# Optimization experiments

Measured on AMD Instinct MI355X. Metric: run time of the kernel, lower is better.

The kernel has to match this reference:

```python
import jax, jax.numpy as jnp
import numpy as np

# dims: B batch, T spikes, X/Y output grid, IN input neurons (weights rows), H hidden neurons
B, T, X, Y = 16, 128, 16, 16
IN_DIM, H_DIM = 256, 64


def setup_inputs() -> dict:
    key = jax.random.key(0)
    k1, k2, k3, k4, k5 = jax.random.split(key, 5)
    inp = {}
    # input only determines batch size in the custom forward (used by backward in torch)
    inp["input"] = jax.random.uniform(k1, (B, IN_DIM, X, Y), jnp.float32) + 0.01
    inp["spikes"] = jax.random.randint(k2, (B, T, X, Y), 0, IN_DIM)
    inp["epsilon_xy"] = jax.random.uniform(k3, (IN_DIM, X, Y), jnp.float32) * 0.1 + 0.01
    inp["epsilon_t_0"] = jax.random.uniform(k4, (T,), jnp.float32) * 0.5 + 0.5
    inp["weights"] = jax.random.uniform(k5, (IN_DIM, H_DIM), jnp.float32) + 1e-3
    inp["h_initial"] = jnp.ones((H_DIM,), jnp.float32) / H_DIM
    inp["forgetting_offset"] = jnp.ones((1,), jnp.float32)
    return inp


def _sbs_hdynamics(spikes, epsilon_xy, epsilon_t_0, weights, h_initial, fo):
    # spikes: [B,T,X,Y] int; weights: [IN,H]; epsilon_xy: [IN,X,Y]; h_initial: [H]
    b, t, x, y = spikes.shape
    h = weights.shape[1]
    xg = jnp.arange(x)[None, :, None]  # broadcast index grids for [B,X,Y] gathers
    yg = jnp.arange(y)[None, None, :]
    fo_per_neuron = fo / h
    h0 = jnp.broadcast_to(h_initial, (b, x, y, h)).astype(weights.dtype)

    def step(h_state, inp):
        sp, eps_t = inp                      # sp: [B,X,Y], eps_t: scalar
        w = weights[sp]                      # [B,X,Y,H] gather of weight rows
        eps = epsilon_xy[sp, xg, yg] * eps_t # [B,X,Y] per-pixel/spike epsilon
        h_temp = h_state * w                 # [B,X,Y,H]
        s = h_temp.sum(axis=-1)              # [B,X,Y]
        safe_s = jnp.where(s > 1e-10, s, 1.0)
        scale = (eps / safe_s)[..., None]
        # h <- (h + eps*h*w/ (h.w) + eps*fo/H) / (1 + eps*(1+fo))  (fo=0 reduces to h/(1+eps))
        upd = (h_state + scale * h_temp + (eps * fo_per_neuron)[..., None]) / (
            1.0 + (eps * (1.0 + fo))[..., None]
        )
        h_new = jnp.where((s > 1e-10)[..., None], upd, h_state)
        return h_new, None

    spikes_t = jnp.transpose(spikes, (1, 0, 2, 3))  # [T,B,X,Y]
    h_final, _ = jax.lax.scan(step, h0, (spikes_t, epsilon_t_0))
    return jnp.transpose(h_final, (0, 3, 1, 2))  # [B,H,X,Y]


def reference(input, spikes, epsilon_xy, epsilon_t_0, weights, h_initial, forgetting_offset):
    fo = forgetting_offset[0]
    return _sbs_hdynamics(spikes, epsilon_xy, epsilon_t_0, weights, h_initial, fo)
```

## Files before the change

kernel.cpp:

```cpp
#include <hip/hip_runtime.h>

#define BB      16
#define TT      128
#define XDIM    16
#define YDIM    16
#define IN_DIM  256
#define H_DIM   64
#define XY      (XDIM*YDIM)


#define DPP_ADD(v, ctrl)                                                      \
    v += __int_as_float(__builtin_amdgcn_update_dpp(                          \
        0, __float_as_int(v), (ctrl), 0xf, 0xf, true))

__global__ __launch_bounds__(256) void sbs_scan_kernel(
    const int*   __restrict__ spikes,
    const float* __restrict__ eps_xy,
    const float* __restrict__ eps_t,
    const float* __restrict__ weights,
    const float* __restrict__ h_init,
    const float* __restrict__ fo_ptr,
    float*       __restrict__ out)
{
    __shared__ int    s_spk[YDIM][TT];
    __shared__ float2 s_P[YDIM][TT];
    __shared__ float  s_out[YDIM][H_DIM];

    const int tid = threadIdx.x;
    const int bi  = blockIdx.x;
    const int b   = bi >> 4;
    const int x   = bi & 15;

    int spv[8];
    #pragma unroll
    for (int k = 0; k < 8; ++k) {
        const int idx = tid + k * 256;
        const int t = idx >> 4, yy = idx & 15;
        const int sp = spikes[(b * TT + t) * XY + x * YDIM + yy];
        spv[k] = sp;
        s_spk[yy][t] = sp;
    }

    const float fo   = fo_ptr[0];
    const float fo1  = 1.0f + fo;
    const float fo_h = fo * (1.0f / (float)H_DIM);

    #pragma unroll
    for (int k = 0; k < 8; ++k) {
        const int idx = tid + k * 256;
        const int t = idx >> 4, yy = idx & 15;
        const float eps = eps_xy[spv[k] * XY + x * YDIM + yy] * eps_t[t];
        const float den = fmaf(eps, fo1, 1.0f);
        float rd = __builtin_amdgcn_rcpf(den);
        rd = fmaf(rd, fmaf(-den, rd, 1.0f), rd);
        s_P[yy][t] = make_float2(rd, eps * rd);
    }
    __syncthreads();

    const int wave = tid >> 6;
    const int lane = tid & 63;
    const int row  = lane >> 4;
    const int il   = lane & 15;
    const int y    = wave * 4 + row;

    const float4* __restrict__ w4 = (const float4*)weights;
    float4 h = ((const float4*)h_init)[il];

    int    sq0 = s_spk[y][3];
    int    sq1 = s_spk[y][4];
    float4 wq0 = w4[s_spk[y][0] * 16 + il];
    float4 wq1 = w4[s_spk[y][1] * 16 + il];
    float4 wq2 = w4[s_spk[y][2] * 16 + il];
    float2 pq0 = s_P[y][0];
    float2 pq1 = s_P[y][1];

    #pragma unroll 4
    for (int t = 0; t < TT; ++t) {
        const int    sq_n = s_spk[y][(t + 5) & (TT - 1)];
        const float4 wq_n = w4[sq0 * 16 + il];
        const float2 pq_n = s_P[y][(t + 2) & (TT - 1)];

        const float ht0 = h.x * wq0.x;
        const float ht1 = h.y * wq0.y;
        const float ht2 = h.z * wq0.z;
        const float ht3 = h.w * wq0.w;
        float r = (ht0 + ht1) + (ht2 + ht3);
        DPP_ADD(r, 0xB1);
        DPP_ADD(r, 0x4E);
        DPP_ADD(r, 0x124);
        DPP_ADD(r, 0x128);
        const float s = r;

        float rs = __builtin_amdgcn_rcpf(s);
        rs = fmaf(rs, fmaf(-s, rs, 1.0f), rs);

        const float rd   = pq0.x;
        const float erd  = pq0.y;
        const float erdf = erd * fo_h;
        const float k2   = erd * rs;
        const float u0 = fmaf(k2, ht0, fmaf(h.x, rd, erdf));
        const float u1 = fmaf(k2, ht1, fmaf(h.y, rd, erdf));
        const float u2 = fmaf(k2, ht2, fmaf(h.z, rd, erdf));
        const float u3 = fmaf(k2, ht3, fmaf(h.w, rd, erdf));
        const bool ok = (s > 1e-10f);
        h.x = ok ? u0 : h.x;
        h.y = ok ? u1 : h.y;
        h.z = ok ? u2 : h.z;
        h.w = ok ? u3 : h.w;

        sq0 = sq1; sq1 = sq_n;
        wq0 = wq1; wq1 = wq2; wq2 = wq_n;
        pq0 = pq1; pq1 = pq_n;
    }

    *(float4*)&s_out[y][4 * il] = h;
    __syncthreads();
    #pragma unroll
    for (int k = 0; k < 4; ++k) {
        const int idx = tid + k * 256;
        const int hh = idx >> 4, yy = idx & 15;
        out[b * (H_DIM * XY) + hh * XY + x * YDIM + yy] = s_out[yy][hh];
    }
}

extern "C" void kernel_launch(void* const* d_in, const int* in_sizes, int n_in,
                              void* d_out, int out_size, void* d_ws, size_t ws_size,
                              hipStream_t stream) {
    const int*   spikes  = (const int*)  d_in[1];
    const float* eps_xy  = (const float*)d_in[2];
    const float* eps_t   = (const float*)d_in[3];
    const float* weights = (const float*)d_in[4];
    const float* h_init  = (const float*)d_in[5];
    const float* fo_ptr  = (const float*)d_in[6];
    float*       out     = (float*)d_out;

    const int grid = BB * XDIM;
    sbs_scan_kernel<<<grid, 256, 0, stream>>>(
        spikes, eps_xy, eps_t, weights, h_init, fo_ptr, out);
}
```

Before: 82.25 us.

## Shorten scan critical path: precompute off-chain terms, drop guard and Newton step

Restructures the per-step update so that everything independent of the reduced sum is computed before the DPP reduction, leaving only one rcp and four FMAs after it. It also removes the Newton refinement of the reciprocal and the s>1e-10 guard, which depends on inputs being positive. In addition it deepens the weight-gather prefetch by one step and pads the shared arrays to avoid bank conflicts. Dropping the guard and refinement slightly changes precision and makes the kernel rely on the sum never being near zero.

```diff
diff --git a/kernel.cpp b/kernel.cpp
--- a/kernel.cpp
+++ b/kernel.cpp
@@ -22,9 +22,9 @@
     const float* __restrict__ fo_ptr,
     float*       __restrict__ out)
 {
-    __shared__ int    s_spk[YDIM][TT];
-    __shared__ float2 s_P[YDIM][TT];
-    __shared__ float  s_out[YDIM][H_DIM];
+    __shared__ int    s_spk[YDIM][TT + 1];
+    __shared__ float2 s_P[YDIM][TT + 1];
+    __shared__ float  s_out[YDIM][H_DIM + 1];
 
     const int tid = threadIdx.x;
     const int bi  = blockIdx.x;
@@ -66,51 +66,54 @@
     const float4* __restrict__ w4 = (const float4*)weights;
     float4 h = ((const float4*)h_init)[il];
 
-    int    sq0 = s_spk[y][3];
-    int    sq1 = s_spk[y][4];
+    int    sq0 = s_spk[y][4];
+    int    sq1 = s_spk[y][5];
     float4 wq0 = w4[s_spk[y][0] * 16 + il];
     float4 wq1 = w4[s_spk[y][1] * 16 + il];
     float4 wq2 = w4[s_spk[y][2] * 16 + il];
+    float4 wq3 = w4[s_spk[y][3] * 16 + il];
     float2 pq0 = s_P[y][0];
     float2 pq1 = s_P[y][1];
+    float2 pq2 = s_P[y][2];
 
     #pragma unroll 4
     for (int t = 0; t < TT; ++t) {
-        const int    sq_n = s_spk[y][(t + 5) & (TT - 1)];
+        const int    sq_n = s_spk[y][(t + 6) & (TT - 1)];
         const float4 wq_n = w4[sq0 * 16 + il];
-        const float2 pq_n = s_P[y][(t + 2) & (TT - 1)];
+        const float2 pq_n = s_P[y][(t + 3) & (TT - 1)];
 
         const float ht0 = h.x * wq0.x;
         const float ht1 = h.y * wq0.y;
         const float ht2 = h.z * wq0.z;
         const float ht3 = h.w * wq0.w;
         float r = (ht0 + ht1) + (ht2 + ht3);
+
+        const float rd   = pq0.x;
+        const float erd  = pq0.y;
+        const float erdf = erd * fo_h;
+        const float eht0 = erd * ht0;
+        const float eht1 = erd * ht1;
+        const float eht2 = erd * ht2;
+        const float eht3 = erd * ht3;
+        const float t30 = fmaf(h.x, rd, erdf);
+        const float t31 = fmaf(h.y, rd, erdf);
+        const float t32 = fmaf(h.z, rd, erdf);
+        const float t33 = fmaf(h.w, rd, erdf);
+
         DPP_ADD(r, 0xB1);
         DPP_ADD(r, 0x4E);
         DPP_ADD(r, 0x124);
         DPP_ADD(r, 0x128);
-        const float s = r;
 
-        float rs = __builtin_amdgcn_rcpf(s);
-        rs = fmaf(rs, fmaf(-s, rs, 1.0f), rs);
-
-        const float rd   = pq0.x;
-        const float erd  = pq0.y;
-        const float erdf = erd * fo_h;
-        const float k2   = erd * rs;
-        const float u0 = fmaf(k2, ht0, fmaf(h.x, rd, erdf));
-        const float u1 = fmaf(k2, ht1, fmaf(h.y, rd, erdf));
-        const float u2 = fmaf(k2, ht2, fmaf(h.z, rd, erdf));
-        const float u3 = fmaf(k2, ht3, fmaf(h.w, rd, erdf));
-        const bool ok = (s > 1e-10f);
-        h.x = ok ? u0 : h.x;
-        h.y = ok ? u1 : h.y;
-        h.z = ok ? u2 : h.z;
-        h.w = ok ? u3 : h.w;
+        const float rs = __builtin_amdgcn_rcpf(r);
+        h.x = fmaf(rs, eht0, t30);
+        h.y = fmaf(rs, eht1, t31);
+        h.z = fmaf(rs, eht2, t32);
+        h.w = fmaf(rs, eht3, t33);
 
         sq0 = sq1; sq1 = sq_n;
-        wq0 = wq1; wq1 = wq2; wq2 = wq_n;
-        pq0 = pq1; pq1 = pq_n;
+        wq0 = wq1; wq1 = wq2; wq2 = wq3; wq3 = wq_n;
+        pq0 = pq1; pq1 = pq2; pq2 = pq_n;
     }
 
     *(float4*)&s_out[y][4 * il] = h;
```

Result: faster. 80.57 us (-2.0%).
